# Kernel optimization log

Hardware: AMD Instinct MI355X
Metric: run time of the kernel (lower is better)

## Reference

```python
import jax, jax.numpy as jnp
import numpy as np

TOPK = 2048


def setup_inputs() -> dict:
    key = jax.random.key(0)
    ks = jax.random.split(key, 16)
    M = 20000
    boxes = jax.random.uniform(ks[0], (M, 4), dtype=jnp.float32)
    scores = jax.random.uniform(ks[1], (M,), dtype=jnp.float32)
    classes = jax.random.randint(ks[2], (M,), 0, 80, dtype=jnp.int64)
    def lin(k, fan_in, fan_out):
        b = 1.0 / np.sqrt(fan_in)
        kw, kb = jax.random.split(k)
        w = jax.random.uniform(kw, (fan_in, fan_out), jnp.float32, -b, b)
        bias = jax.random.uniform(kb, (fan_out,), jnp.float32, -b, b)
        return w, bias
    sup_w1, sup_b1 = lin(ks[3], 7, 32)
    sup_w2, sup_b2 = lin(ks[4], 32, 16)
    sup_w3, sup_b3 = lin(ks[5], 16, 1)
    lam_w1, lam_b1 = lin(ks[6], 5, 16)
    lam_w2, lam_b2 = lin(ks[7], 16, 1)
    return {
        'boxes': boxes, 'scores': scores, 'classes': classes,
        'sup_w1': sup_w1, 'sup_b1': sup_b1, 'sup_w2': sup_w2, 'sup_b2': sup_b2,
        'sup_w3': sup_w3, 'sup_b3': sup_b3,
        'lam_w1': lam_w1, 'lam_b1': lam_b1, 'lam_w2': lam_w2, 'lam_b2': lam_b2,
    }


def _box_iou(b):
    # b: [N,4] in (x, y, w, h)
    x, y, w, h = b[:, 0], b[:, 1], b[:, 2], b[:, 3]
    area = w * h
    ix1 = jnp.maximum(x[:, None], x[None, :])
    iy1 = jnp.maximum(y[:, None], y[None, :])
    ix2 = jnp.minimum((x + w)[:, None], (x + w)[None, :])
    iy2 = jnp.minimum((y + h)[:, None], (y + h)[None, :])
    inter = jnp.clip(ix2 - ix1, 0) * jnp.clip(iy2 - iy1, 0)
    union = area[:, None] + area[None, :] - inter
    return inter / (union + 1e-06)


def _dacs(boxes, scores, classes,
          sup_w1, sup_b1, sup_w2, sup_b2, sup_w3, sup_b3,
          lam_w1, lam_b1, lam_w2, lam_b2):
    k = min(TOPK, scores.shape[0])
    top_scores, idx = jax.lax.top_k(scores, k)
    b = boxes[idx]            # [N,4]
    cls = classes[idx]        # [N]
    N = k
    iou = _box_iou(b)         # [N,N]
    D = iou.mean(axis=1)      # [N]
    x, y, w, h = b[:, 0], b[:, 1], b[:, 2], b[:, 3]
    feats = jnp.stack([
        iou,
        jnp.abs(x[:, None] - x[None, :]),
        jnp.abs(y[:, None] - y[None, :]),
        jnp.abs(w[:, None] - w[None, :]),
        jnp.abs(h[:, None] - h[None, :]),
        jnp.broadcast_to(top_scores[:, None], (N, N)),
        jnp.broadcast_to(top_scores[None, :], (N, N)),
    ], axis=-1)               # [N,N,7]
    hdn = jax.nn.relu(feats @ sup_w1 + sup_b1)       # [N,N,32]
    hdn = jax.nn.relu(hdn @ sup_w2 + sup_b2)         # [N,N,16]
    s_ij = jax.nn.sigmoid((hdn @ sup_w3 + sup_b3)[..., 0])  # [N,N]
    class_mask = (cls[:, None] == cls[None, :]).astype(s_ij.dtype)
    s_ij = s_ij * class_mask
    lam_in = jnp.concatenate([b, top_scores[:, None]], axis=1)  # [N,5]
    lam_h = jax.nn.relu(lam_in @ lam_w1 + lam_b1)
    lam = jax.nn.sigmoid((lam_h @ lam_w2 + lam_b2)[:, 0])       # [N]
    S = jnp.sum(s_ij * iou, axis=1)
    E = lam * S * D
    new_scores = top_scores * jnp.exp(-E)
    return b, new_scores, cls


def reference(boxes, scores, classes,
              sup_w1, sup_b1, sup_w2, sup_b2, sup_w3, sup_b3,
              lam_w1, lam_b1, lam_w2, lam_b2):
    return _dacs(boxes, scores, classes,
                 sup_w1, sup_b1, sup_w2, sup_b2, sup_w3, sup_b3,
                 lam_w1, lam_b1, lam_w2, lam_b2)
```

## Files before the change

### kernel.cpp

```cpp
#include <hip/hip_runtime.h>
#include <math.h>

#define TOPK 2048
#define NCLS 80
#define NBIN 4096
#define CMAX 2560
#define SMAX 20480
#define K1B  32
#define STN  1024
#define CTN  256
#define CROWS 8

struct SelP {
    const float* scores; const float* boxes; const int* classes;
    int M; int K;
    float4* sel_box; float* sel_score; int* sel_cls;
};

struct CmpP {
    const float4* sel_box; const float* sel_score; const int* sel_cls;
    const float* sw1; const float* sb1; const float* sw2; const float* sb2;
    const float* sw3; const float* sb3;
    const float* lw1; const float* lb1; const float* lw2; const float* lb2;
    int K;
    float* out_boxes; float* out_scores; float* out_cls;
};

__device__ __forceinline__ float iou_of(float xi, float yi, float ai,
                                        float x2i, float y2i, float4 bj) {
    float ix1 = fmaxf(xi, bj.x), iy1 = fmaxf(yi, bj.y);
    float ix2 = fminf(x2i, bj.x + bj.z), iy2 = fminf(y2i, bj.y + bj.w);
    float iw = fmaxf(ix2 - ix1, 0.0f), ih = fmaxf(iy2 - iy1, 0.0f);
    float inter = iw * ih;
    float uni = ai + bj.z * bj.w - inter;
    return inter / (uni + 1e-6f);
}

__device__ __forceinline__ int digest12(float s) {
    int v = (int)(s * 4096.0f);
    return v < 0 ? 0 : (v > NBIN - 1 ? NBIN - 1 : v);
}

__device__ __forceinline__ float key_score(unsigned long long kk) {
    unsigned mono = (unsigned)(kk >> 32);
    unsigned ob = (mono & 0x80000000u) ? (mono & 0x7FFFFFFFu) : ~mono;
    return __uint_as_float(ob);
}

__global__ __launch_bounds__(STN, 1) void k_sel(SelP p) {
    __shared__ float ssc[SMAX];
    __shared__ int   bincur[NBIN];
    __shared__ int   binbase[NBIN];
    __shared__ unsigned long long skeys[CMAX];
    __shared__ int   sfx[STN];
    __shared__ int   wsum[STN / 64];
    __shared__ int   sh_cT;

    int tid = threadIdx.x, bid = blockIdx.x;
    int M = p.M, K = p.K, M4 = M >> 2;

    for (int b = tid; b < NBIN; b += STN) bincur[b] = 0;
    __syncthreads();

    const float4* s4p = (const float4*)p.scores;
    for (int i4 = tid; i4 < M4; i4 += STN) {
        float4 v = s4p[i4];
        if (i4 < SMAX / 4) ((float4*)ssc)[i4] = v;
        atomicAdd(&bincur[digest12(v.x)], 1);
        atomicAdd(&bincur[digest12(v.y)], 1);
        atomicAdd(&bincur[digest12(v.z)], 1);
        atomicAdd(&bincur[digest12(v.w)], 1);
    }
    for (int i = M4 * 4 + tid; i < M; i += STN) {
        float s = p.scores[i];
        if (i < SMAX) ssc[i] = s;
        atomicAdd(&bincur[digest12(s)], 1);
    }
    __syncthreads();

    {
        const int BPT = NBIN / STN;
        int c0 = tid * BPT, sum = 0;
        #pragma unroll
        for (int u = 0; u < BPT; u++) sum += bincur[c0 + u];
        int lane = tid & 63;
        int x = sum;
        #pragma unroll
        for (int off = 1; off < 64; off <<= 1) {
            int v = __shfl_down(x, off, 64);
            if (lane + off < 64) x += v;
        }
        if (lane == 0) wsum[tid >> 6] = x;
        __syncthreads();
        if (tid < STN / 64) {
            int t = wsum[tid];
            #pragma unroll
            for (int off = 1; off < STN / 64; off <<= 1) {
                int v = __shfl_down(t, off, 64);
                if (tid + off < STN / 64) t += v;
            }
            wsum[tid] = t;
        }
        __syncthreads();
        int wid = tid >> 6;
        int higher = (wid < STN / 64 - 1) ? wsum[wid + 1] : 0;
        sfx[tid] = x + higher;
    }
    __syncthreads();

    {
        const int BPT = NBIN / STN;
        int running = (tid < STN - 1) ? sfx[tid + 1] : 0;
        int c0 = tid * BPT;
        for (int u = BPT - 1; u >= 0; u--) {
            int b = c0 + u, cnt = bincur[b];
            binbase[b] = running;
            if (running < K && running + cnt >= K) sh_cT = b;
            running += cnt;
        }
    }
    __syncthreads();
    int cT = sh_cT;
    for (int b = tid; b < NBIN; b += STN) bincur[b] = binbase[b];
    __syncthreads();

    for (int i = tid; i < M; i += STN) {
        float s = (i < SMAX) ? ssc[i] : p.scores[i];
        int d = digest12(s);
        if (d >= cT) {
            int slot = atomicAdd(&bincur[d], 1);
            if (slot < CMAX) {
                unsigned b = __float_as_uint(s);
                b = (b & 0x80000000u) ? ~b : (b | 0x80000000u);
                skeys[slot] = ((unsigned long long)b << 32) |
                              (unsigned long long)(0xFFFFFFFFu - (unsigned)i);
            }
        }
    }
    __syncthreads();

    {
        int C = bincur[cT]; if (C > CMAX) C = CMAX;
        const float4* boxes4 = (const float4*)p.boxes;
        for (int s = tid; s < C; s += STN) {
            unsigned long long ks = skeys[s];
            unsigned idx = 0xFFFFFFFFu - (unsigned)(ks & 0xFFFFFFFFull);
            if ((int)(idx & (K1B - 1)) != bid) continue;
            float sc = key_score(ks);
            int d = digest12(sc);
            int st = binbase[d], en = bincur[d]; if (en > CMAX) en = CMAX;
            int r = binbase[d];
            for (int t = st; t < en; t++) r += (skeys[t] > ks) ? 1 : 0;
            if (r < K) {
                p.sel_box[r] = boxes4[idx];
                p.sel_score[r] = sc;
                p.sel_cls[r] = p.classes[idx];
            }
        }
    }
}

__global__ __launch_bounds__(CTN, 1) void k_cmp(CmpP p) {
    __shared__ float4 sbox[TOPK];
    __shared__ float  sscore[TOPK];
    __shared__ short  scls[TOPK];
    __shared__ short  clist[TOPK];
    __shared__ int    ccnt[NCLS], ccur[NCLS], cstart[NCLS + 1];
    __shared__ float  swt[914];
    __shared__ int    prefix[CROWS + 1];
    __shared__ int    rowcs[CROWS];
    __shared__ float  Ssum[CROWS], Drow[CROWS];

    int tid = threadIdx.x, bid = blockIdx.x;
    int K = p.K;

    for (int r = tid; r < K; r += CTN) {
        sbox[r] = p.sel_box[r];
        sscore[r] = p.sel_score[r];
        scls[r] = (short)p.sel_cls[r];
    }

    for (int t = tid; t < 224; t += CTN) swt[t] = p.sw1[t];
    if (tid < 32) swt[224 + tid] = p.sb1[tid];
    for (int t = tid; t < 512; t += CTN) swt[256 + t] = p.sw2[t];
    if (tid < 16) swt[768 + tid] = p.sb2[tid];
    if (tid < 16) swt[784 + tid] = p.sw3[tid];
    if (tid == 0) swt[800] = p.sb3[0];
    if (tid < 80) swt[801 + tid] = p.lw1[tid];
    if (tid < 16) swt[881 + tid] = p.lb1[tid];
    if (tid < 16) swt[897 + tid] = p.lw2[tid];
    if (tid == 0) swt[913] = p.lb2[0];
    if (tid < NCLS) ccnt[tid] = 0;
    __syncthreads();

    for (int r = tid; r < K; r += CTN) atomicAdd(&ccnt[scls[r]], 1);
    __syncthreads();
    if (tid < NCLS) {
        int acc = 0;
        for (int u = 0; u < tid; u++) acc += ccnt[u];
        cstart[tid] = acc;
        ccur[tid] = acc;
    }
    if (tid == 0) cstart[NCLS] = K;
    __syncthreads();
    for (int r = tid; r < K; r += CTN) {
        int pos = atomicAdd(&ccur[scls[r]], 1);
        clist[pos] = (short)r;
    }

    int r0 = bid * CROWS;
    int nrows = K - r0; if (nrows > CROWS) nrows = CROWS;
    if (nrows <= 0) return;
    if (tid < nrows) Ssum[tid] = 0.0f;
    __syncthreads();

    {
        int row = tid >> 5, sub = tid & 31;
        if (row < nrows) {
            float4 bi = sbox[r0 + row];
            float ai = bi.z * bi.w, x2i = bi.x + bi.z, y2i = bi.y + bi.w;
            float dsum = 0.0f;
            for (int j = sub; j < K; j += 32)
                dsum += iou_of(bi.x, bi.y, ai, x2i, y2i, sbox[j]);
            #pragma unroll
            for (int off = 16; off >= 1; off >>= 1)
                dsum += __shfl_xor(dsum, off, 64);
            if (sub == 0) Drow[row] = dsum / (float)K;
        }
    }

    if (tid == 0) {
        int acc = 0;
        for (int rr = 0; rr < nrows; rr++) {
            int c = scls[r0 + rr];
            prefix[rr] = acc;
            rowcs[rr] = cstart[c];
            acc += ccnt[c];
        }
        prefix[nrows] = acc;
    }
    __syncthreads();
    int Pb = prefix[nrows];

    const float* W1 = swt;       const float* B1 = swt + 224;
    const float* W2 = swt + 256; const float* B2 = swt + 768;
    const float* W3 = swt + 784; float B3 = swt[800];

    for (int pp = tid; pp < Pb; pp += CTN) {
        int lo = 0, hi = nrows;
        while (hi - lo > 1) {
            int mid = (lo + hi) >> 1;
            if (prefix[mid] <= pp) lo = mid; else hi = mid;
        }
        int row = lo;
        int j = clist[rowcs[row] + (pp - prefix[row])];
        float4 bi = sbox[r0 + row], bj = sbox[j];
        float ai = bi.z * bi.w, x2i = bi.x + bi.z, y2i = bi.y + bi.w;
        float iou = iou_of(bi.x, bi.y, ai, x2i, y2i, bj);
        float f1 = fabsf(bi.x - bj.x), f2 = fabsf(bi.y - bj.y);
        float f3 = fabsf(bi.z - bj.z), f4 = fabsf(bi.w - bj.w);
        float f5 = sscore[r0 + row], f6 = sscore[j];
        float h[32];
        #pragma unroll
        for (int o = 0; o < 32; o++) {
            float a = B1[o];
            a += iou * W1[0 * 32 + o];
            a += f1 * W1[1 * 32 + o];
            a += f2 * W1[2 * 32 + o];
            a += f3 * W1[3 * 32 + o];
            a += f4 * W1[4 * 32 + o];
            a += f5 * W1[5 * 32 + o];
            a += f6 * W1[6 * 32 + o];
            h[o] = fmaxf(a, 0.0f);
        }
        float acc3 = B3;
        #pragma unroll
        for (int q = 0; q < 16; q++) {
            float a = B2[q];
            #pragma unroll
            for (int o = 0; o < 32; o++) a += h[o] * W2[o * 16 + q];
            acc3 += fmaxf(a, 0.0f) * W3[q];
        }
        atomicAdd(&Ssum[row], iou / (1.0f + expf(-acc3)));
    }
    __syncthreads();

    if (tid < nrows) {
        int r = r0 + tid;
        float4 bi = sbox[r];
        float si = sscore[r];
        const float* LW1 = swt + 801; const float* LB1 = swt + 881;
        const float* LW2 = swt + 897; float LB2 = swt[913];
        float in5[5] = { bi.x, bi.y, bi.z, bi.w, si };
        float acc = LB2;
        #pragma unroll
        for (int o = 0; o < 16; o++) {
            float a2 = LB1[o];
            #pragma unroll
            for (int f = 0; f < 5; f++) a2 += in5[f] * LW1[f * 16 + o];
            acc += fmaxf(a2, 0.0f) * LW2[o];
        }
        float lam = 1.0f / (1.0f + expf(-acc));
        ((float4*)p.out_boxes)[r] = bi;
        p.out_cls[r] = (float)scls[r];
        p.out_scores[r] = si * expf(-lam * Ssum[tid] * Drow[tid]);
    }
}

extern "C" void kernel_launch(void* const* d_in, const int* in_sizes, int n_in,
                              void* d_out, int out_size, void* d_ws, size_t ws_size,
                              hipStream_t stream) {
    int M = in_sizes[1];
    int K = (M < TOPK) ? M : TOPK;

    char* ws = (char*)d_ws;
    float4* sel_box   = (float4*)ws;           ws += (size_t)TOPK * 16;
    float*  sel_score = (float*)ws;            ws += (size_t)TOPK * 4;
    int*    sel_cls   = (int*)ws;              ws += (size_t)TOPK * 4;

    SelP sp;
    sp.scores  = (const float*)d_in[1];
    sp.boxes   = (const float*)d_in[0];
    sp.classes = (const int*)d_in[2];
    sp.M = M; sp.K = K;
    sp.sel_box = sel_box; sp.sel_score = sel_score; sp.sel_cls = sel_cls;

    CmpP cp;
    cp.sel_box = sel_box; cp.sel_score = sel_score; cp.sel_cls = sel_cls;
    cp.sw1 = (const float*)d_in[3];  cp.sb1 = (const float*)d_in[4];
    cp.sw2 = (const float*)d_in[5];  cp.sb2 = (const float*)d_in[6];
    cp.sw3 = (const float*)d_in[7];  cp.sb3 = (const float*)d_in[8];
    cp.lw1 = (const float*)d_in[9];  cp.lb1 = (const float*)d_in[10];
    cp.lw2 = (const float*)d_in[11]; cp.lb2 = (const float*)d_in[12];
    cp.K = K;
    cp.out_boxes  = (float*)d_out;
    cp.out_scores = (float*)d_out + (size_t)K * 4;
    cp.out_cls    = (float*)d_out + (size_t)K * 5;

    k_sel<<<K1B, STN, 0, stream>>>(sp);
    k_cmp<<<(K + CROWS - 1) / CROWS, CTN, 0, stream>>>(cp);
}
```

Measured before the change: 111.1 us.

## Hoist class bucketing into prep kernel and shrink per-block row count

Moves the per-class counting and bucketing, which every compute block used to redo, into a single-block prep kernel that writes cstart and clist to workspace. Compute blocks no longer stage all boxes, scores and classes into shared memory; they read them from global memory (likely L2-resident) and handle 2 rows instead of 8. That gives four times as many blocks, raises occupancy via launch bounds, and fuses MLP layers 1 and 2 so the 32-wide hidden array is never materialised. The cost is an extra kernel launch plus more scattered global reads in the inner loop.

```diff
diff --git a/kernel.cpp b/kernel.cpp
--- a/kernel.cpp
+++ b/kernel.cpp
@@ -8,8 +8,9 @@
 #define SMAX 20480
 #define K1B  32
 #define STN  1024
+#define PTN  1024
 #define CTN  256
-#define CROWS 8
+#define CROWS 2
 
 struct SelP {
     const float* scores; const float* boxes; const int* classes;
@@ -17,8 +18,16 @@
     float4* sel_box; float* sel_score; int* sel_cls;
 };
 
+struct PreP {
+    const int* sel_cls;
+    int K;
+    int* cstart;
+    short* clist;
+};
+
 struct CmpP {
     const float4* sel_box; const float* sel_score; const int* sel_cls;
+    const int* cstart; const short* clist;
     const float* sw1; const float* sb1; const float* sw2; const float* sb2;
     const float* sw3; const float* sb3;
     const float* lw1; const float* lb1; const float* lw2; const float* lb2;
@@ -160,25 +169,57 @@
     }
 }
 
-__global__ __launch_bounds__(CTN, 1) void k_cmp(CmpP p) {
-    __shared__ float4 sbox[TOPK];
-    __shared__ float  sscore[TOPK];
-    __shared__ short  scls[TOPK];
-    __shared__ short  clist[TOPK];
-    __shared__ int    ccnt[NCLS], ccur[NCLS], cstart[NCLS + 1];
-    __shared__ float  swt[914];
-    __shared__ int    prefix[CROWS + 1];
-    __shared__ int    rowcs[CROWS];
-    __shared__ float  Ssum[CROWS], Drow[CROWS];
+__global__ __launch_bounds__(PTN, 1) void k_prep(PreP p) {
+    __shared__ int ccnt[NCLS];
+    __shared__ int ccur[NCLS];
+    __shared__ int wtot;
+
+    int tid = threadIdx.x;
+    int K = p.K;
+    if (tid < NCLS) ccnt[tid] = 0;
+    __syncthreads();
+
+    for (int r = tid; r < K; r += PTN) atomicAdd(&ccnt[p.sel_cls[r]], 1);
+    __syncthreads();
+
+    int x = 0, v = 0;
+    if (tid < 128) {
+        v = (tid < NCLS) ? ccnt[tid] : 0;
+        x = v;
+        #pragma unroll
+        for (int off = 1; off < 64; off <<= 1) {
+            int t = __shfl_up(x, off, 64);
+            if ((tid & 63) >= off) x += t;
+        }
+        if (tid == 63) wtot = x;
+    }
+    __syncthreads();
+    if (tid < NCLS) {
+        int excl = x - v + ((tid >= 64) ? wtot : 0);
+        ccur[tid] = excl;
+        p.cstart[tid] = excl;
+    }
+    if (tid == 0) p.cstart[NCLS] = K;
+    __syncthreads();
+
+    for (int r = tid; r < K; r += PTN) {
+        int pos = atomicAdd(&ccur[p.sel_cls[r]], 1);
+        p.clist[pos] = (short)r;
+    }
+}
+
+__global__ __launch_bounds__(CTN, 4) void k_cmp(CmpP p) {
+    __shared__ float swt[914];
+    __shared__ float wpart[4];
+    __shared__ int   rowc[CROWS];
+    __shared__ int   prefix[CROWS + 1];
+    __shared__ float Ssum[CROWS], Drow[CROWS];
 
     int tid = threadIdx.x, bid = blockIdx.x;
     int K = p.K;
-
-    for (int r = tid; r < K; r += CTN) {
-        sbox[r] = p.sel_box[r];
-        sscore[r] = p.sel_score[r];
-        scls[r] = (short)p.sel_cls[r];
-    }
+    int r0 = bid * CROWS;
+    int nrows = K - r0; if (nrows > CROWS) nrows = CROWS;
+    if (nrows <= 0) return;
 
     for (int t = tid; t < 224; t += CTN) swt[t] = p.sw1[t];
     if (tid < 32) swt[224 + tid] = p.sb1[tid];
@@ -190,77 +231,60 @@
     if (tid < 16) swt[881 + tid] = p.lb1[tid];
     if (tid < 16) swt[897 + tid] = p.lw2[tid];
     if (tid == 0) swt[913] = p.lb2[0];
-    if (tid < NCLS) ccnt[tid] = 0;
-    __syncthreads();
-
-    for (int r = tid; r < K; r += CTN) atomicAdd(&ccnt[scls[r]], 1);
-    __syncthreads();
-    if (tid < NCLS) {
-        int acc = 0;
-        for (int u = 0; u < tid; u++) acc += ccnt[u];
-        cstart[tid] = acc;
-        ccur[tid] = acc;
-    }
-    if (tid == 0) cstart[NCLS] = K;
-    __syncthreads();
-    for (int r = tid; r < K; r += CTN) {
-        int pos = atomicAdd(&ccur[scls[r]], 1);
-        clist[pos] = (short)r;
-    }
-
-    int r0 = bid * CROWS;
-    int nrows = K - r0; if (nrows > CROWS) nrows = CROWS;
-    if (nrows <= 0) return;
-    if (tid < nrows) Ssum[tid] = 0.0f;
-    __syncthreads();
+
+    if (tid < CROWS) {
+        Ssum[tid] = 0.0f;
+        int st = 0, cnt = 0;
+        if (tid < nrows) {
+            int c = p.sel_cls[r0 + tid];
+            st = p.cstart[c];
+            cnt = p.cstart[c + 1] - st;
+        }
+        rowc[tid] = st;
+        prefix[tid] = cnt;
+    }
+    __syncthreads();
+    if (tid == 0) {
+        int a0 = prefix[0], a1 = prefix[1];
+        prefix[0] = 0; prefix[1] = a0; prefix[2] = a0 + a1;
+    }
 
     {
-        int row = tid >> 5, sub = tid & 31;
+        int wv = tid >> 6, lane = tid & 63;
+        int row = wv >> 1, half = wv & 1;
+        float dsum = 0.0f;
         if (row < nrows) {
-            float4 bi = sbox[r0 + row];
+            float4 bi = p.sel_box[r0 + row];
             float ai = bi.z * bi.w, x2i = bi.x + bi.z, y2i = bi.y + bi.w;
-            float dsum = 0.0f;
-            for (int j = sub; j < K; j += 32)
-                dsum += iou_of(bi.x, bi.y, ai, x2i, y2i, sbox[j]);
+            for (int j = lane + (half << 6); j < K; j += 128)
+                dsum += iou_of(bi.x, bi.y, ai, x2i, y2i, p.sel_box[j]);
             #pragma unroll
-            for (int off = 16; off >= 1; off >>= 1)
+            for (int off = 32; off >= 1; off >>= 1)
                 dsum += __shfl_xor(dsum, off, 64);
-            if (sub == 0) Drow[row] = dsum / (float)K;
-        }
-    }
-
-    if (tid == 0) {
-        int acc = 0;
-        for (int rr = 0; rr < nrows; rr++) {
-            int c = scls[r0 + rr];
-            prefix[rr] = acc;
-            rowcs[rr] = cstart[c];
-            acc += ccnt[c];
-        }
-        prefix[nrows] = acc;
-    }
-    __syncthreads();
-    int Pb = prefix[nrows];
-
+        }
+        if (lane == 0) wpart[wv] = dsum;
+    }
+    __syncthreads();
+    if (tid < nrows) Drow[tid] = (wpart[2 * tid] + wpart[2 * tid + 1]) / (float)K;
+
+    int Pb = prefix[CROWS];
     const float* W1 = swt;       const float* B1 = swt + 224;
     const float* W2 = swt + 256; const float* B2 = swt + 768;
     const float* W3 = swt + 784; float B3 = swt[800];
 
     for (int pp = tid; pp < Pb; pp += CTN) {
-        int lo = 0, hi = nrows;
-        while (hi - lo > 1) {
-            int mid = (lo + hi) >> 1;
-            if (prefix[mid] <= pp) lo = mid; else hi = mid;
-        }
-        int row = lo;
-        int j = clist[rowcs[row] + (pp - prefix[row])];
-        float4 bi = sbox[r0 + row], bj = sbox[j];
+        int row = (pp >= prefix[1]) ? 1 : 0;
+        int j = (int)p.clist[rowc[row] + (pp - prefix[row])];
+        float4 bi = p.sel_box[r0 + row];
+        float4 bj = p.sel_box[j];
         float ai = bi.z * bi.w, x2i = bi.x + bi.z, y2i = bi.y + bi.w;
         float iou = iou_of(bi.x, bi.y, ai, x2i, y2i, bj);
         float f1 = fabsf(bi.x - bj.x), f2 = fabsf(bi.y - bj.y);
         float f3 = fabsf(bi.z - bj.z), f4 = fabsf(bi.w - bj.w);
-        float f5 = sscore[r0 + row], f6 = sscore[j];
-        float h[32];
+        float f5 = p.sel_score[r0 + row], f6 = p.sel_score[j];
+        float acc2[16];
+        #pragma unroll
+        for (int q = 0; q < 16; q++) acc2[q] = B2[q];
         #pragma unroll
         for (int o = 0; o < 32; o++) {
             float a = B1[o];
@@ -271,24 +295,21 @@
             a += f4 * W1[4 * 32 + o];
             a += f5 * W1[5 * 32 + o];
             a += f6 * W1[6 * 32 + o];
-            h[o] = fmaxf(a, 0.0f);
+            float h = fmaxf(a, 0.0f);
+            #pragma unroll
+            for (int q = 0; q < 16; q++) acc2[q] += h * W2[o * 16 + q];
         }
         float acc3 = B3;
         #pragma unroll
-        for (int q = 0; q < 16; q++) {
-            float a = B2[q];
-            #pragma unroll
-            for (int o = 0; o < 32; o++) a += h[o] * W2[o * 16 + q];
-            acc3 += fmaxf(a, 0.0f) * W3[q];
-        }
+        for (int q = 0; q < 16; q++) acc3 += fmaxf(acc2[q], 0.0f) * W3[q];
         atomicAdd(&Ssum[row], iou / (1.0f + expf(-acc3)));
     }
     __syncthreads();
 
     if (tid < nrows) {
         int r = r0 + tid;
-        float4 bi = sbox[r];
-        float si = sscore[r];
+        float4 bi = p.sel_box[r];
+        float si = p.sel_score[r];
         const float* LW1 = swt + 801; const float* LB1 = swt + 881;
         const float* LW2 = swt + 897; float LB2 = swt[913];
         float in5[5] = { bi.x, bi.y, bi.z, bi.w, si };
@@ -302,7 +323,7 @@
         }
         float lam = 1.0f / (1.0f + expf(-acc));
         ((float4*)p.out_boxes)[r] = bi;
-        p.out_cls[r] = (float)scls[r];
+        p.out_cls[r] = (float)p.sel_cls[r];
         p.out_scores[r] = si * expf(-lam * Ssum[tid] * Drow[tid]);
     }
 }
@@ -317,6 +338,8 @@
     float4* sel_box   = (float4*)ws;           ws += (size_t)TOPK * 16;
     float*  sel_score = (float*)ws;            ws += (size_t)TOPK * 4;
     int*    sel_cls   = (int*)ws;              ws += (size_t)TOPK * 4;
+    int*    cstart    = (int*)ws;              ws += (size_t)(NCLS + 2) * 4;
+    short*  clist     = (short*)ws;            ws += (size_t)TOPK * 2;
 
     SelP sp;
     sp.scores  = (const float*)d_in[1];
@@ -325,8 +348,13 @@
     sp.M = M; sp.K = K;
     sp.sel_box = sel_box; sp.sel_score = sel_score; sp.sel_cls = sel_cls;
 
+    PreP pp;
+    pp.sel_cls = sel_cls; pp.K = K;
+    pp.cstart = cstart; pp.clist = clist;
+
     CmpP cp;
     cp.sel_box = sel_box; cp.sel_score = sel_score; cp.sel_cls = sel_cls;
+    cp.cstart = cstart; cp.clist = clist;
     cp.sw1 = (const float*)d_in[3];  cp.sb1 = (const float*)d_in[4];
     cp.sw2 = (const float*)d_in[5];  cp.sb2 = (const float*)d_in[6];
     cp.sw3 = (const float*)d_in[7];  cp.sb3 = (const float*)d_in[8];
@@ -338,5 +366,6 @@
     cp.out_cls    = (float*)d_out + (size_t)K * 5;
 
     k_sel<<<K1B, STN, 0, stream>>>(sp);
+    k_prep<<<1, PTN, 0, stream>>>(pp);
     k_cmp<<<(K + CROWS - 1) / CROWS, CTN, 0, stream>>>(cp);
 }
```

Result: slower. 152.8 us (+37.5%).

## Fuse top-k selection and pairwise scoring into one kernel with redundant per-block selection

Applied to the files above, without the earlier changes.

Merges the selection and compute kernels into one launch. Every one of the 256 blocks now redoes the full histogram top-k over all 20000 scores and writes the selected boxes straight into shared memory, which removes the global workspace round trip and the second launch. It also restructures the per-pair MLP to accumulate the 16 second-layer outputs on the fly instead of keeping a 32-entry hidden array, replaces the serial class prefix sum with a wave scan, and uses 1024 threads per block. The cost is redundant selection work and extra global score reads in every block, plus higher register pressure and lower occupancy at 1024 threads with a large shared-memory footprint.

```diff
diff --git a/kernel.cpp b/kernel.cpp
--- a/kernel.cpp
+++ b/kernel.cpp
@@ -5,24 +5,15 @@
 #define NCLS 80
 #define NBIN 4096
 #define CMAX 2560
-#define SMAX 20480
-#define K1B  32
-#define STN  1024
-#define CTN  256
+#define TN   1024
 #define CROWS 8
 
-struct SelP {
+struct P {
     const float* scores; const float* boxes; const int* classes;
-    int M; int K;
-    float4* sel_box; float* sel_score; int* sel_cls;
-};
-
-struct CmpP {
-    const float4* sel_box; const float* sel_score; const int* sel_cls;
     const float* sw1; const float* sb1; const float* sw2; const float* sb2;
     const float* sw3; const float* sb3;
     const float* lw1; const float* lb1; const float* lw2; const float* lb2;
-    int K;
+    int M; int K;
     float* out_boxes; float* out_scores; float* out_cls;
 };
 
@@ -47,39 +38,61 @@
     return __uint_as_float(ob);
 }
 
-__global__ __launch_bounds__(STN, 1) void k_sel(SelP p) {
-    __shared__ float ssc[SMAX];
+__global__ __launch_bounds__(TN, 1) void k_dacs(P p) {
     __shared__ int   bincur[NBIN];
     __shared__ int   binbase[NBIN];
     __shared__ unsigned long long skeys[CMAX];
-    __shared__ int   sfx[STN];
-    __shared__ int   wsum[STN / 64];
+    __shared__ int   sfx[TN];
+    __shared__ int   wsum[TN / 64];
     __shared__ int   sh_cT;
+    __shared__ float4 sbox[TOPK];
+    __shared__ float  sscore[TOPK];
+    __shared__ short  scls[TOPK];
+    __shared__ short  clist[TOPK];
+    __shared__ int    ccnt[NCLS], ccur[NCLS], cstart[NCLS + 1];
+    __shared__ int    wtot;
+    __shared__ float  swt[914];
+    __shared__ float  wpart[TN / 64];
+    __shared__ int    rowc[CROWS];
+    __shared__ int    prefix[CROWS + 1];
+    __shared__ float  Ssum[CROWS], Drow[CROWS];
 
     int tid = threadIdx.x, bid = blockIdx.x;
     int M = p.M, K = p.K, M4 = M >> 2;
-
-    for (int b = tid; b < NBIN; b += STN) bincur[b] = 0;
+    int r0 = bid * CROWS;
+    int nrows = K - r0; if (nrows > CROWS) nrows = CROWS;
+    if (nrows <= 0) return;
+
+    for (int t = tid; t < 224; t += TN) swt[t] = p.sw1[t];
+    if (tid < 32) swt[224 + tid] = p.sb1[tid];
+    for (int t = tid; t < 512; t += TN) swt[256 + t] = p.sw2[t];
+    if (tid < 16) swt[768 + tid] = p.sb2[tid];
+    if (tid < 16) swt[784 + tid] = p.sw3[tid];
+    if (tid == 0) swt[800] = p.sb3[0];
+    if (tid < 80) swt[801 + tid] = p.lw1[tid];
+    if (tid < 16) swt[881 + tid] = p.lb1[tid];
+    if (tid < 16) swt[897 + tid] = p.lw2[tid];
+    if (tid == 0) swt[913] = p.lb2[0];
+
+    for (int b = tid; b < NBIN; b += TN) bincur[b] = 0;
+    if (tid < NCLS) ccnt[tid] = 0;
+    if (tid < CROWS) Ssum[tid] = 0.0f;
     __syncthreads();
 
     const float4* s4p = (const float4*)p.scores;
-    for (int i4 = tid; i4 < M4; i4 += STN) {
+    for (int i4 = tid; i4 < M4; i4 += TN) {
         float4 v = s4p[i4];
-        if (i4 < SMAX / 4) ((float4*)ssc)[i4] = v;
         atomicAdd(&bincur[digest12(v.x)], 1);
         atomicAdd(&bincur[digest12(v.y)], 1);
         atomicAdd(&bincur[digest12(v.z)], 1);
         atomicAdd(&bincur[digest12(v.w)], 1);
     }
-    for (int i = M4 * 4 + tid; i < M; i += STN) {
-        float s = p.scores[i];
-        if (i < SMAX) ssc[i] = s;
-        atomicAdd(&bincur[digest12(s)], 1);
-    }
-    __syncthreads();
-
-    {
-        const int BPT = NBIN / STN;
+    for (int i = M4 * 4 + tid; i < M; i += TN)
+        atomicAdd(&bincur[digest12(p.scores[i])], 1);
+    __syncthreads();
+
+    {
+        const int BPT = NBIN / TN;
         int c0 = tid * BPT, sum = 0;
         #pragma unroll
         for (int u = 0; u < BPT; u++) sum += bincur[c0 + u];
@@ -92,25 +105,25 @@
         }
         if (lane == 0) wsum[tid >> 6] = x;
         __syncthreads();
-        if (tid < STN / 64) {
+        if (tid < TN / 64) {
             int t = wsum[tid];
             #pragma unroll
-            for (int off = 1; off < STN / 64; off <<= 1) {
+            for (int off = 1; off < TN / 64; off <<= 1) {
                 int v = __shfl_down(t, off, 64);
-                if (tid + off < STN / 64) t += v;
+                if (tid + off < TN / 64) t += v;
             }
             wsum[tid] = t;
         }
         __syncthreads();
         int wid = tid >> 6;
-        int higher = (wid < STN / 64 - 1) ? wsum[wid + 1] : 0;
+        int higher = (wid < TN / 64 - 1) ? wsum[wid + 1] : 0;
         sfx[tid] = x + higher;
     }
     __syncthreads();
 
     {
-        const int BPT = NBIN / STN;
-        int running = (tid < STN - 1) ? sfx[tid + 1] : 0;
+        const int BPT = NBIN / TN;
+        int running = (tid < TN - 1) ? sfx[tid + 1] : 0;
         int c0 = tid * BPT;
         for (int u = BPT - 1; u >= 0; u--) {
             int b = c0 + u, cnt = bincur[b];
@@ -121,11 +134,29 @@
     }
     __syncthreads();
     int cT = sh_cT;
-    for (int b = tid; b < NBIN; b += STN) bincur[b] = binbase[b];
-    __syncthreads();
-
-    for (int i = tid; i < M; i += STN) {
-        float s = (i < SMAX) ? ssc[i] : p.scores[i];
+    for (int b = tid; b < NBIN; b += TN) bincur[b] = binbase[b];
+    __syncthreads();
+
+    for (int i4 = tid; i4 < M4; i4 += TN) {
+        float4 v = s4p[i4];
+        #pragma unroll
+        for (int u = 0; u < 4; u++) {
+            float s = (u == 0) ? v.x : (u == 1) ? v.y : (u == 2) ? v.z : v.w;
+            int d = digest12(s);
+            if (d >= cT) {
+                int i = i4 * 4 + u;
+                int slot = atomicAdd(&bincur[d], 1);
+                if (slot < CMAX) {
+                    unsigned b = __float_as_uint(s);
+                    b = (b & 0x80000000u) ? ~b : (b | 0x80000000u);
+                    skeys[slot] = ((unsigned long long)b << 32) |
+                                  (unsigned long long)(0xFFFFFFFFu - (unsigned)i);
+                }
+            }
+        }
+    }
+    for (int i = M4 * 4 + tid; i < M; i += TN) {
+        float s = p.scores[i];
         int d = digest12(s);
         if (d >= cT) {
             int slot = atomicAdd(&bincur[d], 1);
@@ -139,129 +170,115 @@
     }
     __syncthreads();
 
-    {
-        int C = bincur[cT]; if (C > CMAX) C = CMAX;
+    int C = bincur[cT]; if (C > CMAX) C = CMAX;
+    {
         const float4* boxes4 = (const float4*)p.boxes;
-        for (int s = tid; s < C; s += STN) {
+        for (int s = tid; s < C; s += TN) {
             unsigned long long ks = skeys[s];
             unsigned idx = 0xFFFFFFFFu - (unsigned)(ks & 0xFFFFFFFFull);
-            if ((int)(idx & (K1B - 1)) != bid) continue;
             float sc = key_score(ks);
             int d = digest12(sc);
             int st = binbase[d], en = bincur[d]; if (en > CMAX) en = CMAX;
             int r = binbase[d];
             for (int t = st; t < en; t++) r += (skeys[t] > ks) ? 1 : 0;
             if (r < K) {
-                p.sel_box[r] = boxes4[idx];
-                p.sel_score[r] = sc;
-                p.sel_cls[r] = p.classes[idx];
-            }
-        }
-    }
-}
-
-__global__ __launch_bounds__(CTN, 1) void k_cmp(CmpP p) {
-    __shared__ float4 sbox[TOPK];
-    __shared__ float  sscore[TOPK];
-    __shared__ short  scls[TOPK];
-    __shared__ short  clist[TOPK];
-    __shared__ int    ccnt[NCLS], ccur[NCLS], cstart[NCLS + 1];
-    __shared__ float  swt[914];
-    __shared__ int    prefix[CROWS + 1];
-    __shared__ int    rowcs[CROWS];
-    __shared__ float  Ssum[CROWS], Drow[CROWS];
-
-    int tid = threadIdx.x, bid = blockIdx.x;
-    int K = p.K;
-
-    for (int r = tid; r < K; r += CTN) {
-        sbox[r] = p.sel_box[r];
-        sscore[r] = p.sel_score[r];
-        scls[r] = (short)p.sel_cls[r];
-    }
-
-    for (int t = tid; t < 224; t += CTN) swt[t] = p.sw1[t];
-    if (tid < 32) swt[224 + tid] = p.sb1[tid];
-    for (int t = tid; t < 512; t += CTN) swt[256 + t] = p.sw2[t];
-    if (tid < 16) swt[768 + tid] = p.sb2[tid];
-    if (tid < 16) swt[784 + tid] = p.sw3[tid];
-    if (tid == 0) swt[800] = p.sb3[0];
-    if (tid < 80) swt[801 + tid] = p.lw1[tid];
-    if (tid < 16) swt[881 + tid] = p.lb1[tid];
-    if (tid < 16) swt[897 + tid] = p.lw2[tid];
-    if (tid == 0) swt[913] = p.lb2[0];
-    if (tid < NCLS) ccnt[tid] = 0;
-    __syncthreads();
-
-    for (int r = tid; r < K; r += CTN) atomicAdd(&ccnt[scls[r]], 1);
-    __syncthreads();
-    if (tid < NCLS) {
-        int acc = 0;
-        for (int u = 0; u < tid; u++) acc += ccnt[u];
-        cstart[tid] = acc;
-        ccur[tid] = acc;
-    }
-    if (tid == 0) cstart[NCLS] = K;
-    __syncthreads();
-    for (int r = tid; r < K; r += CTN) {
-        int pos = atomicAdd(&ccur[scls[r]], 1);
-        clist[pos] = (short)r;
-    }
-
-    int r0 = bid * CROWS;
-    int nrows = K - r0; if (nrows > CROWS) nrows = CROWS;
-    if (nrows <= 0) return;
-    if (tid < nrows) Ssum[tid] = 0.0f;
-    __syncthreads();
-
-    {
-        int row = tid >> 5, sub = tid & 31;
+                sbox[r] = boxes4[idx];
+                sscore[r] = sc;
+                scls[r] = (short)p.classes[idx];
+            }
+        }
+    }
+    __syncthreads();
+
+    for (int r = tid; r < K; r += TN) atomicAdd(&ccnt[scls[r]], 1);
+    __syncthreads();
+    {
+        int x = 0, v = 0;
+        if (tid < 128) {
+            v = (tid < NCLS) ? ccnt[tid] : 0;
+            x = v;
+            #pragma unroll
+            for (int off = 1; off < 64; off <<= 1) {
+                int t = __shfl_up(x, off, 64);
+                if ((tid & 63) >= off) x += t;
+            }
+            if (tid == 63) wtot = x;
+        }
+        __syncthreads();
+        if (tid < NCLS) {
+            int excl = x - v + ((tid >= 64) ? wtot : 0);
+            ccur[tid] = excl;
+            cstart[tid] = excl;
+        }
+        if (tid == 0) cstart[NCLS] = K;
+        __syncthreads();
+        for (int r = tid; r < K; r += TN) {
+            int pos = atomicAdd(&ccur[scls[r]], 1);
+            clist[pos] = (short)r;
+        }
+    }
+    __syncthreads();
+
+    {
+        int wv = tid >> 6, lane = tid & 63;
+        int row = wv >> 1, half = wv & 1;
+        float dsum = 0.0f;
         if (row < nrows) {
             float4 bi = sbox[r0 + row];
             float ai = bi.z * bi.w, x2i = bi.x + bi.z, y2i = bi.y + bi.w;
-            float dsum = 0.0f;
-            for (int j = sub; j < K; j += 32)
+            for (int j = lane + (half << 6); j < K; j += 128)
                 dsum += iou_of(bi.x, bi.y, ai, x2i, y2i, sbox[j]);
             #pragma unroll
-            for (int off = 16; off >= 1; off >>= 1)
+            for (int off = 32; off >= 1; off >>= 1)
                 dsum += __shfl_xor(dsum, off, 64);
-            if (sub == 0) Drow[row] = dsum / (float)K;
-        }
-    }
-
+        }
+        if (lane == 0) wpart[wv] = dsum;
+    }
+
+    if (tid < CROWS) {
+        int st = 0, cnt = 0;
+        if (tid < nrows) {
+            int c = scls[r0 + tid];
+            st = cstart[c];
+            cnt = cstart[c + 1] - st;
+        }
+        rowc[tid] = st;
+        prefix[tid] = cnt;
+    }
+    __syncthreads();
+    if (tid < nrows) Drow[tid] = (wpart[2 * tid] + wpart[2 * tid + 1]) / (float)K;
     if (tid == 0) {
         int acc = 0;
-        for (int rr = 0; rr < nrows; rr++) {
-            int c = scls[r0 + rr];
-            prefix[rr] = acc;
-            rowcs[rr] = cstart[c];
-            acc += ccnt[c];
-        }
-        prefix[nrows] = acc;
-    }
-    __syncthreads();
-    int Pb = prefix[nrows];
-
+        #pragma unroll
+        for (int rr = 0; rr < CROWS; rr++) { int t = prefix[rr]; prefix[rr] = acc; acc += t; }
+        prefix[CROWS] = acc;
+    }
+    __syncthreads();
+
+    int Pb = prefix[CROWS];
     const float* W1 = swt;       const float* B1 = swt + 224;
     const float* W2 = swt + 256; const float* B2 = swt + 768;
     const float* W3 = swt + 784; float B3 = swt[800];
 
-    for (int pp = tid; pp < Pb; pp += CTN) {
-        int lo = 0, hi = nrows;
+    for (int pp = tid; pp < Pb; pp += TN) {
+        int lo = 0, hi = CROWS;
         while (hi - lo > 1) {
             int mid = (lo + hi) >> 1;
             if (prefix[mid] <= pp) lo = mid; else hi = mid;
         }
         int row = lo;
-        int j = clist[rowcs[row] + (pp - prefix[row])];
-        float4 bi = sbox[r0 + row], bj = sbox[j];
+        int j = (int)clist[rowc[row] + (pp - prefix[row])];
+        float4 bi = sbox[r0 + row];
+        float4 bj = sbox[j];
         float ai = bi.z * bi.w, x2i = bi.x + bi.z, y2i = bi.y + bi.w;
         float iou = iou_of(bi.x, bi.y, ai, x2i, y2i, bj);
         float f1 = fabsf(bi.x - bj.x), f2 = fabsf(bi.y - bj.y);
         float f3 = fabsf(bi.z - bj.z), f4 = fabsf(bi.w - bj.w);
         float f5 = sscore[r0 + row], f6 = sscore[j];
-        float h[32];
-        #pragma unroll
+        float acc2[16];
+        #pragma unroll
+        for (int q = 0; q < 16; q++) acc2[q] = B2[q];
+        #pragma unroll 2
         for (int o = 0; o < 32; o++) {
             float a = B1[o];
             a += iou * W1[0 * 32 + o];
@@ -271,16 +288,13 @@
             a += f4 * W1[4 * 32 + o];
             a += f5 * W1[5 * 32 + o];
             a += f6 * W1[6 * 32 + o];
-            h[o] = fmaxf(a, 0.0f);
+            float h = fmaxf(a, 0.0f);
+            #pragma unroll
+            for (int q = 0; q < 16; q++) acc2[q] += h * W2[o * 16 + q];
         }
         float acc3 = B3;
         #pragma unroll
-        for (int q = 0; q < 16; q++) {
-            float a = B2[q];
-            #pragma unroll
-            for (int o = 0; o < 32; o++) a += h[o] * W2[o * 16 + q];
-            acc3 += fmaxf(a, 0.0f) * W3[q];
-        }
+        for (int q = 0; q < 16; q++) acc3 += fmaxf(acc2[q], 0.0f) * W3[q];
         atomicAdd(&Ssum[row], iou / (1.0f + expf(-acc3)));
     }
     __syncthreads();
@@ -313,30 +327,20 @@
     int M = in_sizes[1];
     int K = (M < TOPK) ? M : TOPK;
 
-    char* ws = (char*)d_ws;
-    float4* sel_box   = (float4*)ws;           ws += (size_t)TOPK * 16;
-    float*  sel_score = (float*)ws;            ws += (size_t)TOPK * 4;
-    int*    sel_cls   = (int*)ws;              ws += (size_t)TOPK * 4;
-
-    SelP sp;
-    sp.scores  = (const float*)d_in[1];
-    sp.boxes   = (const float*)d_in[0];
-    sp.classes = (const int*)d_in[2];
-    sp.M = M; sp.K = K;
-    sp.sel_box = sel_box; sp.sel_score = sel_score; sp.sel_cls = sel_cls;
-
-    CmpP cp;
-    cp.sel_box = sel_box; cp.sel_score = sel_score; cp.sel_cls = sel_cls;
-    cp.sw1 = (const float*)d_in[3];  cp.sb1 = (const float*)d_in[4];
-    cp.sw2 = (const float*)d_in[5];  cp.sb2 = (const float*)d_in[6];
-    cp.sw3 = (const float*)d_in[7];  cp.sb3 = (const float*)d_in[8];
-    cp.lw1 = (const float*)d_in[9];  cp.lb1 = (const float*)d_in[10];
-    cp.lw2 = (const float*)d_in[11]; cp.lb2 = (const float*)d_in[12];
-    cp.K = K;
-    cp.out_boxes  = (float*)d_out;
-    cp.out_scores = (float*)d_out + (size_t)K * 4;
-    cp.out_cls    = (float*)d_out + (size_t)K * 5;
-
-    k_sel<<<K1B, STN, 0, stream>>>(sp);
-    k_cmp<<<(K + CROWS - 1) / CROWS, CTN, 0, stream>>>(cp);
-}
+    P dp;
+    dp.scores  = (const float*)d_in[1];
+    dp.boxes   = (const float*)d_in[0];
+    dp.classes = (const int*)d_in[2];
+    dp.sw1 = (const float*)d_in[3];  dp.sb1 = (const float*)d_in[4];
+    dp.sw2 = (const float*)d_in[5];  dp.sb2 = (const float*)d_in[6];
+    dp.sw3 = (const float*)d_in[7];  dp.sb3 = (const float*)d_in[8];
+    dp.lw1 = (const float*)d_in[9];  dp.lb1 = (const float*)d_in[10];
+    dp.lw2 = (const float*)d_in[11]; dp.lb2 = (const float*)d_in[12];
+    dp.M = M; dp.K = K;
+    dp.out_boxes  = (float*)d_out;
+    dp.out_scores = (float*)d_out + (size_t)K * 4;
+    dp.out_cls    = (float*)d_out + (size_t)K * 5;
+
+    int nb = (K + CROWS - 1) / CROWS;
+    k_dacs<<<nb, TN, 0, stream>>>(dp);
+}
```

After: 102.9 us. -7.4%, faster.
